# Kernel optimization log

Measured on AMD Instinct MI355X. Metric: run time of the kernel, lower is better.

The kernel has to match this reference:

```python
import jax, jax.numpy as jnp
import numpy as np

EMA_DECAY = 0.99
EPS = 1e-05
BETA = 0.25


def setup_inputs() -> dict:
    key = jax.random.key(0)
    k1, k2, k3 = jax.random.split(key, 3)
    inputs = jax.random.normal(k1, (4, 8, 32, 32, 128), dtype=jnp.float32)
    cluster_mean = jax.random.normal(k2, (10000, 128), dtype=jnp.float32)
    cluster_size = jnp.ones((10000,), dtype=jnp.float32)
    cluster_sum = jax.random.normal(k3, (10000, 128), dtype=jnp.float32)
    return {"inputs": inputs, "cluster_mean": cluster_mean,
            "cluster_size": cluster_size, "cluster_sum": cluster_sum}


def reference(inputs, cluster_mean, cluster_size, cluster_sum):
    n_embed, embed_dim = cluster_mean.shape
    samples = inputs.reshape(-1, embed_dim)  # [N, D]
    dist = (jnp.sum(samples ** 2, axis=1, keepdims=True)
            - 2.0 * samples @ cluster_mean.T
            + jnp.sum(cluster_mean ** 2, axis=1)[None, :])
    cluster_index = jnp.argmin(dist, axis=1)  # [N]
    # EMA codebook update (scatter via segment_sum, equivalent to one-hot matmul)
    counts = jax.ops.segment_sum(jnp.ones_like(cluster_index, dtype=jnp.float32),
                                 cluster_index, num_segments=n_embed)
    sums = jax.ops.segment_sum(samples, cluster_index, num_segments=n_embed)
    new_size = cluster_size * EMA_DECAY + counts * (1.0 - EMA_DECAY)
    new_sum = cluster_sum * EMA_DECAY + sums * (1.0 - EMA_DECAY)
    n_sample = jnp.sum(new_size)
    smoothed = (new_size + EPS) * n_sample / (n_sample + n_embed * EPS)
    new_mean = new_sum / smoothed[:, None]  # [K, D]
    # Embedding lookup on the updated codebook (matches TF assign-then-lookup order)
    idx = cluster_index.reshape(inputs.shape[:-1])
    quantize = new_mean[idx]  # gather [B,T,H,W,D]
    e_loss = jnp.mean((inputs - jax.lax.stop_gradient(quantize)) ** 2)
    outputs = inputs + jax.lax.stop_gradient(quantize - inputs)
    return outputs, idx, BETA * e_loss
```

## Files before the change

### kernel.cpp

```cpp
#include <hip/hip_runtime.h>

#define N_SAMPLES 32768
#define N_EMBED   10000
#define KPAD      10240
#define HLEN      5120
#define ITERS     160
#define DIM       128
#define OUT_ELEMS 4194304
#define IDX_OFF   4194304
#define LOSS_OFF  4227072

#define WS_CNH      0u
#define WS_NEWSIZE  65536u
#define WS_SUMS     131072u
#define WS_NSAMPLE  5251072u
#define WS_LOSS     5251080u
#define WS_PACKED   5251088u
#define WS_EHI      6291456u
#define WS_ELO      8912896u

#define ROWB   272
#define LO_OFF 8704
#define BUFSZ  17408

typedef _Float16 f16;
typedef __attribute__((ext_vector_type(8)))  _Float16 f16x8;
typedef __attribute__((ext_vector_type(16))) float    f32x16;

__device__ inline unsigned long long shflx64(unsigned long long v, int m) {
    int lo = __shfl_xor((int)(unsigned int)(v & 0xffffffffull), m, 64);
    int hi = __shfl_xor((int)(unsigned int)(v >> 32), m, 64);
    return ((unsigned long long)(unsigned int)hi << 32) | (unsigned int)lo;
}

__global__ __launch_bounds__(128) void k_prepe(const float* __restrict__ cm,
                                               f16* __restrict__ ehi,
                                               f16* __restrict__ elo,
                                               float* __restrict__ cnh) {
    __shared__ float pw[2];
    int c = blockIdx.x, d = threadIdx.x;
    float e = (c < N_EMBED) ? cm[(size_t)c * DIM + d] : 0.f;
    f16 h = (f16)e;
    ehi[(size_t)c * DIM + d] = h;
    elo[(size_t)c * DIM + d] = (f16)(e - (float)h);
    float s = e * e;
    #pragma unroll
    for (int off = 32; off; off >>= 1) s += __shfl_down(s, off, 64);
    if ((threadIdx.x & 63) == 0) pw[threadIdx.x >> 6] = s;
    __syncthreads();
    if (threadIdx.x == 0)
        cnh[c] = (c < N_EMBED) ? -0.5f * (pw[0] + pw[1]) : -1.5e38f;
}

__global__ __launch_bounds__(256, 2) void k_argmin(const float* __restrict__ inp,
                                                   const f16* __restrict__ ehi,
                                                   const f16* __restrict__ elo,
                                                   const float* __restrict__ cnh,
                                                   unsigned long long* __restrict__ packed) {
    __shared__ __align__(16) char lds[2 * BUFSZ];
    const int tid = threadIdx.x;
    const int wave = tid >> 6, lane = tid & 63;
    const int l31 = lane & 31, h = lane >> 5;
    const int g = blockIdx.x >> 1;
    const int kbase = (blockIdx.x & 1) * HLEN;
    const int sbase = g * 128 + wave * 32;

    f16x8 ah[8], al[8];
    {
        const float* xr = inp + (size_t)(sbase + l31) * DIM + h * 8;
        #pragma unroll
        for (int ks = 0; ks < 8; ++ks) {
            float4 u0 = *(const float4*)(xr + ks * 16);
            float4 u1 = *(const float4*)(xr + ks * 16 + 4);
            float v[8] = {u0.x, u0.y, u0.z, u0.w, u1.x, u1.y, u1.z, u1.w};
            f16x8 hv, lv;
            #pragma unroll
            for (int e = 0; e < 8; ++e) {
                f16 hh = (f16)v[e];
                hv[e] = hh;
                lv[e] = (f16)(v[e] - (float)hh);
            }
            ah[ks] = hv; al[ks] = lv;
        }
    }

    const int rb = l31 * ROWB + h * 16;
    const int strow = tid >> 3;
    const int scp = (tid & 7) * 2;
    const int wadr = strow * ROWB + scp * 16;

    float best[16];
    int bi[16];
    #pragma unroll
    for (int r = 0; r < 16; ++r) { best[r] = -3.4e38f; bi[r] = 0; }

    float cn_cur;
    {
        const size_t gs = (size_t)(kbase + strow) * DIM + scp * 8;
        f16x8 sh0 = *(const f16x8*)(ehi + gs);
        f16x8 sh1 = *(const f16x8*)(ehi + gs + 8);
        f16x8 sl0 = *(const f16x8*)(elo + gs);
        f16x8 sl1 = *(const f16x8*)(elo + gs + 8);
        cn_cur = cnh[kbase + l31];
        *(f16x8*)(lds + wadr)               = sh0;
        *(f16x8*)(lds + wadr + 16)          = sh1;
        *(f16x8*)(lds + LO_OFF + wadr)      = sl0;
        *(f16x8*)(lds + LO_OFF + wadr + 16) = sl1;
        __syncthreads();
    }

    int cur = 0;
    for (int it = 0; it < ITERS; ++it) {
        const int c0 = kbase + it * 32;
        f16x8 sh0, sh1, sl0, sl1; float cn_nx = 0.f;
        if (it < ITERS - 1) {
            const size_t gs = (size_t)(c0 + 32 + strow) * DIM + scp * 8;
            sh0 = *(const f16x8*)(ehi + gs);
            sh1 = *(const f16x8*)(ehi + gs + 8);
            sl0 = *(const f16x8*)(elo + gs);
            sl1 = *(const f16x8*)(elo + gs + 8);
            cn_nx = cnh[c0 + 32 + l31];
        }

        const char* lr = lds + cur * BUFSZ + rb;
        f32x16 acc;
        #pragma unroll
        for (int r = 0; r < 16; ++r) acc[r] = cn_cur;
        #pragma unroll
        for (int ks = 0; ks < 8; ++ks) {
            f16x8 bh = *(const f16x8*)(lr + ks * 32);
            f16x8 bl = *(const f16x8*)(lr + LO_OFF + ks * 32);
            acc = __builtin_amdgcn_mfma_f32_32x32x16_f16(ah[ks], bh, acc, 0, 0, 0);
            acc = __builtin_amdgcn_mfma_f32_32x32x16_f16(ah[ks], bl, acc, 0, 0, 0);
            acc = __builtin_amdgcn_mfma_f32_32x32x16_f16(al[ks], bh, acc, 0, 0, 0);
        }

        const int cv = c0 + l31;
        #pragma unroll
        for (int r = 0; r < 16; ++r) {
            bool gt = acc[r] > best[r];
            best[r] = gt ? acc[r] : best[r];
            bi[r]   = gt ? cv : bi[r];
        }

        if (it < ITERS - 1) {
            char* lw = lds + (cur ^ 1) * BUFSZ;
            *(f16x8*)(lw + wadr)               = sh0;
            *(f16x8*)(lw + wadr + 16)          = sh1;
            *(f16x8*)(lw + LO_OFF + wadr)      = sl0;
            *(f16x8*)(lw + LO_OFF + wadr + 16) = sl1;
            __syncthreads();
            cn_cur = cn_nx;
            cur ^= 1;
        }
    }

    #pragma unroll
    for (int r = 0; r < 16; ++r) {
        unsigned int b = __float_as_uint(best[r]);
        unsigned int t = (b & 0x80000000u) ? ~b : (b | 0x80000000u);
        unsigned long long p = ((unsigned long long)(~t) << 32) | (unsigned int)bi[r];
        #pragma unroll
        for (int m = 1; m < 32; m <<= 1) {
            unsigned long long o = shflx64(p, m);
            p = p < o ? p : o;
        }
        if (l31 == r) {
            const int srow = (r & 3) + 8 * (r >> 2) + 4 * h;
            atomicMin(&packed[sbase + srow], p);
        }
    }
}

__global__ __launch_bounds__(256) void k_scatter(const float* __restrict__ inp,
                                                 const unsigned long long* __restrict__ packed,
                                                 float* __restrict__ sums,
                                                 float* __restrict__ counts,
                                                 float* __restrict__ idxf) {
    int j = blockIdx.x * 256 + threadIdx.x;
    int i = j >> 7, d = j & 127;
    int k = (int)(unsigned int)(packed[i] & 0xFFFFFFFFull);
    atomicAdd(&sums[(size_t)k * DIM + d], inp[j]);
    if (d == 0) {
        atomicAdd(&counts[k], 1.0f);
        idxf[i] = (float)k;
    }
}

__global__ __launch_bounds__(256) void k_newsize(const float* __restrict__ csize,
                                                 float* __restrict__ newsize,
                                                 double* __restrict__ nsample) {
    int k = blockIdx.x * 256 + threadIdx.x;
    float ns = 0.f;
    if (k < N_EMBED) {
        ns = csize[k] * 0.99f + newsize[k] * 0.01f;
        newsize[k] = ns;
    }
    float s = ns;
    #pragma unroll
    for (int off = 32; off; off >>= 1) s += __shfl_down(s, off, 64);
    if ((threadIdx.x & 63) == 0) atomicAdd(nsample, (double)s);
}

__global__ __launch_bounds__(256) void k_newmean(const float* __restrict__ csum,
                                                 float* __restrict__ sums,
                                                 const float* __restrict__ newsize,
                                                 const double* __restrict__ nsample) {
    int j = blockIdx.x * 256 + threadIdx.x;
    float nsmp = (float)(*nsample);
    int k = j >> 7;
    float sm = (newsize[k] + 1e-5f) * nsmp / (nsmp + 0.1f);
    sums[j] = (csum[j] * 0.99f + sums[j] * 0.01f) / sm;
}

__global__ __launch_bounds__(256) void k_gather(const float* __restrict__ inp,
                                                const float* __restrict__ nm,
                                                const unsigned long long* __restrict__ packed,
                                                float* __restrict__ out,
                                                double* __restrict__ lossacc) {
    __shared__ double pw[4];
    int t0 = blockIdx.x * 256 + threadIdx.x;
    double de = 0.0;
    #pragma unroll
    for (int it = 0; it < 8; ++it) {
        int j4 = t0 + it * 131072;
        int i = j4 >> 5, d4 = j4 & 31;
        int k = (int)(unsigned int)(packed[i] & 0xFFFFFFFFull);
        float4 x = ((const float4*)inp)[j4];
        float4 qv = ((const float4*)(nm + (size_t)k * DIM))[d4];
        float4 o;
        o.x = x.x + (qv.x - x.x); o.y = x.y + (qv.y - x.y);
        o.z = x.z + (qv.z - x.z); o.w = x.w + (qv.w - x.w);
        ((float4*)out)[j4] = o;
        float dx = x.x - qv.x, dy = x.y - qv.y, dz = x.z - qv.z, dw = x.w - qv.w;
        de += (double)(dx * dx + dy * dy + dz * dz + dw * dw);
    }
    #pragma unroll
    for (int off = 32; off; off >>= 1) de += __shfl_down(de, off, 64);
    if ((threadIdx.x & 63) == 0) pw[threadIdx.x >> 6] = de;
    __syncthreads();
    if (threadIdx.x == 0)
        atomicAdd(lossacc, pw[0] + pw[1] + pw[2] + pw[3]);
}

__global__ void k_lossfinal(const double* __restrict__ lossacc,
                            float* __restrict__ lossout) {
    *lossout = 0.25f * (float)(*lossacc / (double)OUT_ELEMS);
}

extern "C" void kernel_launch(void* const* d_in, const int* in_sizes, int n_in,
                              void* d_out, int out_size, void* d_ws, size_t ws_size,
                              hipStream_t stream) {
    const float* inp   = (const float*)d_in[0];
    const float* cmean = (const float*)d_in[1];
    const float* csize = (const float*)d_in[2];
    const float* csum  = (const float*)d_in[3];
    float* out = (float*)d_out;
    char*  ws  = (char*)d_ws;

    float*  cnh     = (float*)(ws + WS_CNH);
    float*  newsize = (float*)(ws + WS_NEWSIZE);
    float*  sums    = (float*)(ws + WS_SUMS);
    double* nsample = (double*)(ws + WS_NSAMPLE);
    double* lossacc = (double*)(ws + WS_LOSS);
    unsigned long long* packed = (unsigned long long*)(ws + WS_PACKED);
    f16* ehi = (f16*)(ws + WS_EHI);
    f16* elo = (f16*)(ws + WS_ELO);
    float* idxf = out + IDX_OFF;

    hipMemsetAsync(ws + WS_NEWSIZE, 0, (WS_LOSS + 8) - WS_NEWSIZE, stream);
    hipMemsetAsync(ws + WS_PACKED, 0xFF, (size_t)N_SAMPLES * 8, stream);

    k_prepe  <<<KPAD, 128, 0, stream>>>(cmean, ehi, elo, cnh);
    k_argmin <<<512, 256, 0, stream>>>(inp, ehi, elo, cnh, packed);
    k_scatter<<<OUT_ELEMS / 256, 256, 0, stream>>>(inp, packed, sums, newsize, idxf);
    k_newsize<<<(N_EMBED + 255) / 256, 256, 0, stream>>>(csize, newsize, nsample);
    k_newmean<<<(N_EMBED * DIM) / 256, 256, 0, stream>>>(csum, sums, newsize, nsample);
    k_gather <<<512, 256, 0, stream>>>(inp, sums, packed, out, lossacc);
    k_lossfinal<<<1, 1, 0, stream>>>(lossacc, out + LOSS_OFF);
}
```

Baseline: 353.0 us.

## Stage codebook tiles via direct global-to-LDS loads with XOR swizzle, 64 codes per iteration

The codebook f16 hi/lo arrays are now written in an XOR-swizzled layout by the prep kernel, so they can be copied straight into LDS with global_load_lds, bypassing registers. The LDS reads use matching swizzled addresses to avoid bank conflicts. Each iteration now processes 64 codes as two 32x32 MFMA tiles with interleaved accumulators, which halves the iteration count and the number of barriers. The cost is a 64 KB LDS footprint, which may limit how many blocks fit per CU, and an extra accumulator set that raises register pressure.

```diff
diff --git a/kernel.cpp b/kernel.cpp
--- a/kernel.cpp
+++ b/kernel.cpp
@@ -4,7 +4,7 @@
 #define N_EMBED   10000
 #define KPAD      10240
 #define HLEN      5120
-#define ITERS     160
+#define ITERS     80
 #define DIM       128
 #define OUT_ELEMS 4194304
 #define IDX_OFF   4194304
@@ -19,10 +19,6 @@
 #define WS_EHI      6291456u
 #define WS_ELO      8912896u
 
-#define ROWB   272
-#define LO_OFF 8704
-#define BUFSZ  17408
-
 typedef _Float16 f16;
 typedef __attribute__((ext_vector_type(8)))  _Float16 f16x8;
 typedef __attribute__((ext_vector_type(16))) float    f32x16;
@@ -31,6 +27,12 @@
     int lo = __shfl_xor((int)(unsigned int)(v & 0xffffffffull), m, 64);
     int hi = __shfl_xor((int)(unsigned int)(v >> 32), m, 64);
     return ((unsigned long long)(unsigned int)hi << 32) | (unsigned int)lo;
+}
+
+__device__ __forceinline__ void g2l16(const void* g, void* l) {
+    __builtin_amdgcn_global_load_lds(
+        (const __attribute__((address_space(1))) unsigned int*)g,
+        (__attribute__((address_space(3))) unsigned int*)l, 16, 0, 0);
 }
 
 __global__ __launch_bounds__(128) void k_prepe(const float* __restrict__ cm,
@@ -41,8 +43,10 @@
     int c = blockIdx.x, d = threadIdx.x;
     float e = (c < N_EMBED) ? cm[(size_t)c * DIM + d] : 0.f;
     f16 h = (f16)e;
-    ehi[(size_t)c * DIM + d] = h;
-    elo[(size_t)c * DIM + d] = (f16)(e - (float)h);
+    int ch = d >> 3, e8 = d & 7;
+    size_t pos = (size_t)c * DIM + ((ch ^ (c & 15)) << 3) + e8;
+    ehi[pos] = h;
+    elo[pos] = (f16)(e - (float)h);
     float s = e * e;
     #pragma unroll
     for (int off = 32; off; off >>= 1) s += __shfl_down(s, off, 64);
@@ -57,7 +61,7 @@
                                                    const f16* __restrict__ elo,
                                                    const float* __restrict__ cnh,
                                                    unsigned long long* __restrict__ packed) {
-    __shared__ __align__(16) char lds[2 * BUFSZ];
+    __shared__ __align__(16) char lds[65536];
     const int tid = threadIdx.x;
     const int wave = tid >> 6, lane = tid & 63;
     const int l31 = lane & 31, h = lane >> 5;
@@ -84,73 +88,77 @@
         }
     }
 
-    const int rb = l31 * ROWB + h * 16;
-    const int strow = tid >> 3;
-    const int scp = (tid & 7) * 2;
-    const int wadr = strow * ROWB + scp * 16;
+    int adr[8];
+    {
+        const int km = (l31 >> 1) & 7;
+        const int base = l31 * 256 + ((h ^ (l31 & 1)) << 4);
+        #pragma unroll
+        for (int ks = 0; ks < 8; ++ks) adr[ks] = base | ((ks ^ km) << 5);
+    }
 
     float best[16];
     int bi[16];
     #pragma unroll
     for (int r = 0; r < 16; ++r) { best[r] = -3.4e38f; bi[r] = 0; }
 
-    float cn_cur;
-    {
-        const size_t gs = (size_t)(kbase + strow) * DIM + scp * 8;
-        f16x8 sh0 = *(const f16x8*)(ehi + gs);
-        f16x8 sh1 = *(const f16x8*)(ehi + gs + 8);
-        f16x8 sl0 = *(const f16x8*)(elo + gs);
-        f16x8 sl1 = *(const f16x8*)(elo + gs + 8);
-        cn_cur = cnh[kbase + l31];
-        *(f16x8*)(lds + wadr)               = sh0;
-        *(f16x8*)(lds + wadr + 16)          = sh1;
-        *(f16x8*)(lds + LO_OFF + wadr)      = sl0;
-        *(f16x8*)(lds + LO_OFF + wadr + 16) = sl1;
-        __syncthreads();
-    }
+    auto STAGE = [&](int buf, int c0) {
+        const char* sh = (const char*)ehi + (size_t)c0 * 256 + wave * 4096 + lane * 16;
+        const char* sl = (const char*)elo + (size_t)c0 * 256 + wave * 4096 + lane * 16;
+        char* dh = lds + buf * 32768 + wave * 4096;
+        #pragma unroll
+        for (int j = 0; j < 4; ++j) {
+            g2l16(sh + j * 1024, dh + j * 1024);
+            g2l16(sl + j * 1024, dh + j * 1024 + 16384);
+        }
+    };
+
+    STAGE(0, kbase);
+    float cnA = cnh[kbase + l31], cnB = cnh[kbase + 32 + l31];
+    __syncthreads();
 
     int cur = 0;
     for (int it = 0; it < ITERS; ++it) {
-        const int c0 = kbase + it * 32;
-        f16x8 sh0, sh1, sl0, sl1; float cn_nx = 0.f;
-        if (it < ITERS - 1) {
-            const size_t gs = (size_t)(c0 + 32 + strow) * DIM + scp * 8;
-            sh0 = *(const f16x8*)(ehi + gs);
-            sh1 = *(const f16x8*)(ehi + gs + 8);
-            sl0 = *(const f16x8*)(elo + gs);
-            sl1 = *(const f16x8*)(elo + gs + 8);
-            cn_nx = cnh[c0 + 32 + l31];
-        }
-
-        const char* lr = lds + cur * BUFSZ + rb;
-        f32x16 acc;
-        #pragma unroll
-        for (int r = 0; r < 16; ++r) acc[r] = cn_cur;
+        const int c0 = kbase + it * 64;
+        const bool more = (it < ITERS - 1);
+        float cnA2 = 0.f, cnB2 = 0.f;
+        if (more) {
+            STAGE(cur ^ 1, c0 + 64);
+            cnA2 = cnh[c0 + 64 + l31];
+            cnB2 = cnh[c0 + 96 + l31];
+        }
+
+        const char* lr = lds + cur * 32768;
+        f32x16 aA, aB;
+        #pragma unroll
+        for (int r = 0; r < 16; ++r) { aA[r] = cnA; aB[r] = cnB; }
         #pragma unroll
         for (int ks = 0; ks < 8; ++ks) {
-            f16x8 bh = *(const f16x8*)(lr + ks * 32);
-            f16x8 bl = *(const f16x8*)(lr + LO_OFF + ks * 32);
-            acc = __builtin_amdgcn_mfma_f32_32x32x16_f16(ah[ks], bh, acc, 0, 0, 0);
-            acc = __builtin_amdgcn_mfma_f32_32x32x16_f16(ah[ks], bl, acc, 0, 0, 0);
-            acc = __builtin_amdgcn_mfma_f32_32x32x16_f16(al[ks], bh, acc, 0, 0, 0);
-        }
-
-        const int cv = c0 + l31;
+            f16x8 bhA = *(const f16x8*)(lr + adr[ks]);
+            f16x8 bhB = *(const f16x8*)(lr + adr[ks] + 8192);
+            f16x8 blA = *(const f16x8*)(lr + adr[ks] + 16384);
+            f16x8 blB = *(const f16x8*)(lr + adr[ks] + 24576);
+            aA = __builtin_amdgcn_mfma_f32_32x32x16_f16(ah[ks], bhA, aA, 0, 0, 0);
+            aB = __builtin_amdgcn_mfma_f32_32x32x16_f16(ah[ks], bhB, aB, 0, 0, 0);
+            aA = __builtin_amdgcn_mfma_f32_32x32x16_f16(al[ks], bhA, aA, 0, 0, 0);
+            aB = __builtin_amdgcn_mfma_f32_32x32x16_f16(al[ks], bhB, aB, 0, 0, 0);
+            aA = __builtin_amdgcn_mfma_f32_32x32x16_f16(ah[ks], blA, aA, 0, 0, 0);
+            aB = __builtin_amdgcn_mfma_f32_32x32x16_f16(ah[ks], blB, aB, 0, 0, 0);
+        }
+
+        const int cvA = c0 + l31, cvB = cvA + 32;
         #pragma unroll
         for (int r = 0; r < 16; ++r) {
-            bool gt = acc[r] > best[r];
-            best[r] = gt ? acc[r] : best[r];
-            bi[r]   = gt ? cv : bi[r];
-        }
-
-        if (it < ITERS - 1) {
-            char* lw = lds + (cur ^ 1) * BUFSZ;
-            *(f16x8*)(lw + wadr)               = sh0;
-            *(f16x8*)(lw + wadr + 16)          = sh1;
-            *(f16x8*)(lw + LO_OFF + wadr)      = sl0;
-            *(f16x8*)(lw + LO_OFF + wadr + 16) = sl1;
+            bool gA = aA[r] > best[r];
+            best[r] = gA ? aA[r] : best[r];
+            bi[r]   = gA ? cvA : bi[r];
+            bool gB = aB[r] > best[r];
+            best[r] = gB ? aB[r] : best[r];
+            bi[r]   = gB ? cvB : bi[r];
+        }
+
+        if (more) {
             __syncthreads();
-            cn_cur = cn_nx;
+            cnA = cnA2; cnB = cnB2;
             cur ^= 1;
         }
     }
```

After: 353.0 us. Within noise of the previous version (+0.0%).
